# Kernel tuning notes

Hardware: AMD Instinct MI355X
Metric: run time of the kernel (lower is better)

Reference implementation:

```python
import jax, jax.numpy as jnp
import numpy as np

B, K, D, TPE, PPE, HEADS = 8, 128, 128, 64, 64, 8


def setup_inputs() -> dict:
    key = jax.random.key(0)
    ks = jax.random.split(key, 16)
    rn = lambda i, s: jax.random.normal(ks[i], s, dtype=jnp.float32)
    w = lambda i, s: rn(i, s) * 0.05
    z = lambda n: jnp.zeros((n,), jnp.float32)
    return {
        "v_f": rn(0, (B, K, D)),
        "e_f": rn(1, (B, K * K, D)),
        "p_pe": rn(2, (B, K, PPE)),
        "t_pe": rn(3, (B, TPE)),
        "W_vpe": w(4, (D + PPE + TPE, D)), "b_vpe": z(D),
        "W_epe": w(5, (D + TPE, D)), "b_epe": z(D),
        "W_ev1": w(6, (D + 2 * D, D)), "b_ev1": z(D),
        "W_ev2": w(7, (D, D)), "b_ev2": z(D),
        "W_q": w(8, (D, D)), "b_q": z(D),
        "W_k": w(9, (D, D)), "b_k": z(D),
        "W_self": w(10, (D, D)), "b_self": z(D),
        "W_out": w(11, (2 * D, D)), "b_out": z(D),
    }


def reference(v_f, e_f, p_pe, t_pe, W_vpe, b_vpe, W_epe, b_epe, W_ev1, b_ev1,
              W_ev2, b_ev2, W_q, b_q, W_k, b_k, W_self, b_self, W_out, b_out):
    silu = jax.nn.silu
    Bv, Kv, _ = v_f.shape
    t_dim = t_pe.shape[-1]
    # PE binding MLPs
    t_v = jnp.broadcast_to(t_pe[:, None, :], (Bv, Kv, t_dim))
    v = silu(jnp.concatenate([v_f, p_pe, t_v], -1) @ W_vpe + b_vpe)  # [B,K,D]
    t_e = jnp.broadcast_to(t_pe[:, None, :], (Bv, Kv * Kv, t_dim))
    e = silu(jnp.concatenate([e_f, t_e], -1) @ W_epe + b_epe)        # [B,K*K,D]
    Dv = v.shape[-1]
    # pairwise node features + edge feature -> edge value MLP
    e_mtx = e.reshape(Bv, Kv, Kv, -1)
    ev = jnp.concatenate([
        jnp.broadcast_to(v[:, :, None, :], (Bv, Kv, Kv, Dv)),
        jnp.broadcast_to(v[:, None, :, :], (Bv, Kv, Kv, Dv)),
        e_mtx], -1)                                                   # [B,K,K,3D]
    e_value = silu(ev @ W_ev1 + b_ev1) @ W_ev2 + b_ev2                # [B,K,K,E]
    E = e_value.shape[-1]
    G = E // HEADS
    # grouped-head elementwise-QK attention, softmax over neighbor axis (2)
    q = v @ W_q + b_q
    k = v @ W_k + b_k
    scores = (q[:, :, None, :] * k[:, None, :, :]).reshape(Bv, Kv, Kv, G, HEADS)
    scores = scores.sum(-1) / np.float32(np.sqrt(HEADS * 3.0))        # [B,K,K,G]
    atten = jax.nn.softmax(scores, axis=2)
    agg = (atten[..., None] * e_value.reshape(Bv, Kv, Kv, G, HEADS)).sum(2)
    agg = agg.reshape(Bv, Kv, E)
    vf = agg + silu(v @ W_self + b_self)
    pool = jnp.broadcast_to(vf.max(axis=1, keepdims=True), vf.shape)
    v_out = silu(jnp.concatenate([vf, pool], -1) @ W_out + b_out)     # [B,K,Vout]
    return v_out, e_value.reshape(Bv, Kv * Kv, E)
```

## Files before the change

### kernel.cpp

```cpp
#include <hip/hip_runtime.h>
#include <hip/hip_bf16.h>


typedef __attribute__((ext_vector_type(8)))  short bh8;
typedef __attribute__((ext_vector_type(16))) float f16v;
typedef __attribute__((ext_vector_type(4)))  float f4v;

__device__ __forceinline__ unsigned short f2bf(float f) {
  unsigned u = __builtin_bit_cast(unsigned, f);
  u += 0x7fffu + ((u >> 16) & 1u);
  return (unsigned short)(u >> 16);
}
__device__ __forceinline__ float silu_f(float x) {
  float e = __builtin_amdgcn_exp2f(x * -1.44269504088896f);
  return x * __builtin_amdgcn_rcpf(1.f + e);
}
__device__ __forceinline__ bh8 cvt8(f4v x, f4v y) {
  bh8 a;
  a[0] = (short)f2bf(x[0]); a[1] = (short)f2bf(x[1]);
  a[2] = (short)f2bf(x[2]); a[3] = (short)f2bf(x[3]);
  a[4] = (short)f2bf(y[0]); a[5] = (short)f2bf(y[1]);
  a[6] = (short)f2bf(y[2]); a[7] = (short)f2bf(y[3]);
  return a;
}
typedef const __attribute__((address_space(1))) unsigned int gq_t;
typedef __attribute__((address_space(3))) unsigned int lq_t;
__device__ __forceinline__ void gload_lds16(const void* g, void* l) {
  __builtin_amdgcn_global_load_lds((gq_t*)g, (lq_t*)l, 16, 0, 0);
}

__device__ __forceinline__ void wfrag_work(const float* __restrict__ W,
                                           short* __restrict__ dst, int kdim,
                                           int blk, int nblk) {
  int ksteps = kdim >> 4;
  int total  = kdim * 128;
  for (int idx = blk * 256 + threadIdx.x; idx < total; idx += nblk * 256) {
    int jj = idx & 7;
    int l  = (idx >> 3) & 63;
    int rest = idx >> 9;
    int ks = rest % ksteps;
    int ni = rest / ksteps;
    int n  = ni * 32 + (l & 31);
    int kk = ks * 16 + ((l >> 5) << 3) + jj;
    dst[idx] = (short)f2bf(W[kk * 128 + n]);
  }
}

__global__ __launch_bounds__(256) void k_front(
    const float* __restrict__ W_epe, short* __restrict__ wf1,
    const float* __restrict__ W_ev1, short* __restrict__ wf2,
    const float* __restrict__ W_ev2, short* __restrict__ wf3,
    const float* __restrict__ tpe, const float* __restrict__ bepe,
    float* __restrict__ tc,
    const float* __restrict__ vfeat, const float* __restrict__ ppe,
    const float* __restrict__ Wv, const float* __restrict__ bv,
    const float* __restrict__ Wq, const float* __restrict__ bq,
    const float* __restrict__ Wk, const float* __restrict__ bk,
    const float* __restrict__ Ws, const float* __restrict__ bs,
    const float* __restrict__ We, const float* __restrict__ be,
    unsigned short* __restrict__ vb16, float* __restrict__ q,
    float* __restrict__ kb, float* __restrict__ sa, float* __restrict__ evi) {
  const int blk = blockIdx.x;
  if (blk < 260) {
    if (blk < 64)       wfrag_work(W_epe, wf1, 128, blk, 64);
    else if (blk < 192) wfrag_work(W_ev1 + 128 * 128, wf2, 256, blk - 64, 128);
    else if (blk < 256) wfrag_work(W_ev2, wf3, 128, blk - 192, 64);
    else {
      int t = threadIdx.x;
      int b = (blk - 256) * 2 + (t >> 7);
      int n = t & 127;
      float a = bepe[n];
      for (int k2 = 0; k2 < 64; ++k2)
        a += tpe[b * 64 + k2] * W_epe[(128 + k2) * 128 + n];
      tc[b * 128 + n] = a;
    }
    return;
  }
  __shared__ float x[4][256];
  __shared__ float par[2][4][128];
  __shared__ float xv[4][128];
  const int r0 = (blk - 260) * 4;
  const int b  = r0 >> 7;
  const int t  = threadIdx.x;
  const int c  = t & 127;
  const int hf = t >> 7;
  #pragma unroll
  for (int rr = 0; rr < 4; ++rr) {
    int row = r0 + rr;
    x[rr][t] = (t < 128) ? vfeat[row * 128 + t]
             : (t < 192) ? ppe[row * 64 + (t - 128)]
                         : tpe[b * 64 + (t - 192)];
  }
  __syncthreads();
  {
    float a0 = 0.f, a1 = 0.f, a2 = 0.f, a3 = 0.f;
    const int k0 = hf * 128;
    for (int k4 = k0; k4 < k0 + 128; k4 += 4) {
      f4v x0 = *(const f4v*)&x[0][k4];
      f4v x1 = *(const f4v*)&x[1][k4];
      f4v x2 = *(const f4v*)&x[2][k4];
      f4v x3 = *(const f4v*)&x[3][k4];
      #pragma unroll
      for (int u = 0; u < 4; ++u) {
        float wv = Wv[(k4 + u) * 128 + c];
        a0 += x0[u] * wv; a1 += x1[u] * wv; a2 += x2[u] * wv; a3 += x3[u] * wv;
      }
    }
    par[hf][0][c] = a0; par[hf][1][c] = a1; par[hf][2][c] = a2; par[hf][3][c] = a3;
  }
  __syncthreads();
  if (hf == 0) {
    const float bvv = bv[c];
    #pragma unroll
    for (int rr = 0; rr < 4; ++rr) {
      float s = silu_f(par[0][rr][c] + par[1][rr][c] + bvv);
      vb16[(r0 + rr) * 128 + c] = f2bf(s);
      xv[rr][c] = s;
    }
  }
  __syncthreads();
  const float* WA = hf ? Ws : Wq;
  const float* WB = hf ? We : Wk;
  const float  ba = hf ? bs[c] : bq[c];
  const float  bb = hf ? be[c] : bk[c];
  float aA[4] = {ba, ba, ba, ba}, aB[4] = {bb, bb, bb, bb};
  for (int k4 = 0; k4 < 128; k4 += 4) {
    f4v x0 = *(const f4v*)&xv[0][k4];
    f4v x1 = *(const f4v*)&xv[1][k4];
    f4v x2 = *(const f4v*)&xv[2][k4];
    f4v x3 = *(const f4v*)&xv[3][k4];
    #pragma unroll
    for (int u = 0; u < 4; ++u) {
      float wa = WA[(k4 + u) * 128 + c];
      float wb = WB[(k4 + u) * 128 + c];
      aA[0] += x0[u] * wa; aA[1] += x1[u] * wa; aA[2] += x2[u] * wa; aA[3] += x3[u] * wa;
      aB[0] += x0[u] * wb; aB[1] += x1[u] * wb; aB[2] += x2[u] * wb; aB[3] += x3[u] * wb;
    }
  }
  if (hf == 0) {
    #pragma unroll
    for (int rr = 0; rr < 4; ++rr) {
      q[(r0 + rr) * 128 + c]  = aA[rr];
      kb[(r0 + rr) * 128 + c] = aB[rr];
    }
  } else {
    #pragma unroll
    for (int rr = 0; rr < 4; ++rr) {
      sa[(r0 + rr) * 128 + c]  = silu_f(aA[rr]);
      evi[(r0 + rr) * 128 + c] = aB[rr];
    }
  }
}

__global__ void k_atten(const float* __restrict__ q, const float* __restrict__ kmat,
                        float* __restrict__ atten) {
  __shared__ float qr[128];
  __shared__ float s[128][17];
  __shared__ float red[8][17];
  __shared__ float gmax[16];
  __shared__ float gsum[16];
  const int bi = blockIdx.x;
  const int b  = bi >> 7;
  const int t  = threadIdx.x;
  qr[t] = q[bi * 128 + t];
  __syncthreads();
  const float sc = 0.20412414523193154f;
  float loc[16];
  const float* krow = kmat + (size_t)(b * 128 + t) * 128;
  #pragma unroll
  for (int g = 0; g < 16; ++g) {
    f4v k0 = *(const f4v*)&krow[g * 8];
    f4v k1 = *(const f4v*)&krow[g * 8 + 4];
    float a = 0.f;
    #pragma unroll
    for (int h = 0; h < 4; ++h) a += qr[g * 8 + h] * k0[h] + qr[g * 8 + 4 + h] * k1[h];
    loc[g] = a * sc;
    s[t][g] = loc[g];
  }
  __syncthreads();
  { int g = t & 15, c = t >> 4;
    float m = -1e30f;
    for (int j2 = c * 16; j2 < c * 16 + 16; ++j2) m = fmaxf(m, s[j2][g]);
    red[c][g] = m; }
  __syncthreads();
  if (t < 16) {
    float m = red[0][t];
    #pragma unroll
    for (int c = 1; c < 8; ++c) m = fmaxf(m, red[c][t]);
    gmax[t] = m;
  }
  __syncthreads();
  #pragma unroll
  for (int g = 0; g < 16; ++g) {
    loc[g] = __builtin_amdgcn_exp2f((loc[g] - gmax[g]) * 1.44269504088896f);
    s[t][g] = loc[g];
  }
  __syncthreads();
  { int g = t & 15, c = t >> 4;
    float m = 0.f;
    for (int j2 = c * 16; j2 < c * 16 + 16; ++j2) m += s[j2][g];
    red[c][g] = m; }
  __syncthreads();
  if (t < 16) {
    float m = 0.f;
    #pragma unroll
    for (int c = 0; c < 8; ++c) m += red[c][t];
    gsum[t] = m;
  }
  __syncthreads();
  float* ab = atten + (size_t)bi * 2048 + (size_t)t * 16;
  #pragma unroll
  for (int g = 0; g < 16; ++g) ab[g] = loc[g] * __builtin_amdgcn_rcpf(gsum[g]);
}

__global__ __launch_bounds__(256) void k_edge(
    const float* __restrict__ ef, const unsigned short* __restrict__ vb,
    const short* __restrict__ wf1, const short* __restrict__ wf2,
    const short* __restrict__ wf3, const float* __restrict__ tc,
    const float* __restrict__ evic, const float* __restrict__ bev2,
    const float* __restrict__ atten, const float* __restrict__ sab,
    float* __restrict__ oute, float* __restrict__ vfb) {
  __shared__ __align__(16) unsigned short wbuf0[4096];
  __shared__ __align__(16) unsigned short wbuf1[4096];
  __shared__ __align__(16) unsigned short hbuf[128 * 136];
  const int bi  = blockIdx.x;
  const int b   = bi >> 7;
  const int tid = threadIdx.x;
  const int w   = tid >> 6;
  const int l   = tid & 63;
  const int row = w * 32 + (l & 31);
  const int kh  = (l >> 5) << 3;
  const int cb  = l & 31;
  const int rb  = w * 32 + ((l >> 5) << 2);

  const float* efr = ef + (size_t)(bi * 128 + row) * 128;
  const unsigned short* vj = vb + (size_t)(b * 128 + row) * 128;

  auto stage2 = [&](const short* wfp, int KST, int kc, unsigned short* dstb) {
    #pragma unroll
    for (int it = 0; it < 2; ++it) {
      int g  = it * 4 + w;
      int ni = g & 3, kso = g >> 2;
      const short* src = wfp + ((size_t)(ni * KST + kc * 2 + kso) * 64 + l) * 8;
      gload_lds16(src, dstb + g * 512);
    }
  };
  f16v acc[4];
  auto compute2 = [&](const unsigned short* ws2, bh8 aa, bh8 ab2) {
    #pragma unroll
    for (int ni = 0; ni < 4; ++ni) {
      bh8 b0 = *(const bh8*)&ws2[ni * 512 + l * 8];
      acc[ni] = __builtin_amdgcn_mfma_f32_32x32x16_bf16(aa, b0, acc[ni], 0, 0, 0);
    }
    #pragma unroll
    for (int ni = 0; ni < 4; ++ni) {
      bh8 b1 = *(const bh8*)&ws2[(4 + ni) * 512 + l * 8];
      acc[ni] = __builtin_amdgcn_mfma_f32_32x32x16_bf16(ab2, b1, acc[ni], 0, 0, 0);
    }
  };
  auto ldA = [&](int t) -> bh8 {
    if (t < 8) {
      const float* p = efr + t * 16 + kh;
      f4v x0 = *(const f4v*)p;
      f4v x1 = *(const f4v*)(p + 4);
      return cvt8(x0, x1);
    } else if (t < 16) {
      return *(const bh8*)(vj + (t - 8) * 16 + kh);
    } else if (t < 24) {
      return *(const bh8*)&hbuf[row * 136 + (t - 16) * 16 + kh];
    } else {
      return *(const bh8*)&hbuf[row * 136 + (t - 24) * 16 + kh];
    }
  };

  float tin[4], ein[4];
  #pragma unroll
  for (int ni = 0; ni < 4; ++ni) {
    tin[ni] = tc[b * 128 + ni * 32 + cb];
    ein[ni] = evic[bi * 128 + ni * 32 + cb];
  }
  #pragma unroll
  for (int ni = 0; ni < 4; ++ni)
    #pragma unroll
    for (int r = 0; r < 16; ++r) acc[ni][r] = tin[ni];

  stage2(wf1, 8, 0, wbuf0);
  bh8 a0c = ldA(0), a1c = ldA(1);
  __syncthreads();

  #pragma unroll
  for (int c = 0; c < 16; ++c) {
    if (c + 1 < 16) {
      const short* wp; int KST, kc;
      if (c + 1 < 4)       { wp = wf1; KST = 8;  kc = c + 1; }
      else if (c + 1 < 12) { wp = wf2; KST = 16; kc = c + 1 - 4; }
      else                 { wp = wf3; KST = 8;  kc = c + 1 - 12; }
      stage2(wp, KST, kc, (c & 1) ? wbuf0 : wbuf1);
    }
    bh8 a0n, a1n;
    const bool pre = (c + 1 < 16) && (c != 11);
    if (pre) { a0n = ldA(2 * (c + 1)); a1n = ldA(2 * (c + 1) + 1); }
    compute2((c & 1) ? wbuf1 : wbuf0, a0c, a1c);
    if (c == 3) {
      #pragma unroll
      for (int ni = 0; ni < 4; ++ni) {
        int n = ni * 32 + cb;
        #pragma unroll
        for (int r = 0; r < 16; ++r) {
          int rj = rb + (r & 3) + ((r >> 2) << 3);
          hbuf[rj * 136 + n] = f2bf(silu_f(acc[ni][r]));
          acc[ni][r] = ein[ni];
        }
      }
    }
    if (c == 11) {
      #pragma unroll
      for (int ni = 0; ni < 4; ++ni) {
        int n = ni * 32 + cb;
        #pragma unroll
        for (int r = 0; r < 16; ++r) {
          int rj = rb + (r & 3) + ((r >> 2) << 3);
          hbuf[rj * 136 + n] = f2bf(silu_f(acc[ni][r]));
          acc[ni][r] = 0.f;
        }
      }
      a0c = ldA(24); a1c = ldA(25);
    } else if (pre) {
      a0c = a0n; a1c = a1n;
    }
    __syncthreads();
  }

  #pragma unroll
  for (int ni = 0; ni < 4; ++ni) {
    int n = ni * 32 + cb;
    float bv = bev2[n];
    #pragma unroll
    for (int r = 0; r < 16; ++r) {
      int rj = rb + (r & 3) + ((r >> 2) << 3);
      acc[ni][r] += bv;
      oute[(size_t)(bi * 128 + rj) * 128 + n] = acc[ni][r];
    }
  }

  __syncthreads();
  float* attf = (float*)hbuf;
  float* aggl = attf + 2048;
  const float* ap = atten + (size_t)bi * 2048;
  #pragma unroll
  for (int u = 0; u < 8; ++u) {
    int idx = u * 256 + tid;
    float v = ap[idx];
    int j2 = idx >> 4, g = idx & 15;
    attf[j2 * 16 + (g & 3) * 4 + (g >> 2)] = v;
  }
  float sav = 0.f;
  if (tid < 128) sav = sab[(size_t)bi * 128 + tid];
  __syncthreads();
  float p0 = 0.f, p1 = 0.f, p2 = 0.f, p3 = 0.f;
  const int gl = (l & 31) >> 3;
  #pragma unroll
  for (int r = 0; r < 16; ++r) {
    int rj = rb + (r & 3) + ((r >> 2) << 3);
    f4v av = *(const f4v*)&attf[rj * 16 + gl * 4];
    p0 += av[0] * acc[0][r]; p1 += av[1] * acc[1][r];
    p2 += av[2] * acc[2][r]; p3 += av[3] * acc[3][r];
  }
  p0 += __shfl_xor(p0, 32); p1 += __shfl_xor(p1, 32);
  p2 += __shfl_xor(p2, 32); p3 += __shfl_xor(p3, 32);
  if (l < 32) {
    aggl[w * 128 +  0 + l] = p0;
    aggl[w * 128 + 32 + l] = p1;
    aggl[w * 128 + 64 + l] = p2;
    aggl[w * 128 + 96 + l] = p3;
  }
  __syncthreads();
  if (tid < 128) {
    vfb[(size_t)bi * 128 + tid] =
        aggl[tid] + aggl[128 + tid] + aggl[256 + tid] + aggl[384 + tid] + sav;
  }
}

__global__ void k_pool(const float* __restrict__ vfb, float* __restrict__ pool) {
  const int b = blockIdx.x, t = threadIdx.x;
  float m0 = -1e30f, m1 = -1e30f, m2 = -1e30f, m3 = -1e30f;
  for (int i = 0; i < 128; i += 4) {
    m0 = fmaxf(m0, vfb[(size_t)(b * 128 + i + 0) * 128 + t]);
    m1 = fmaxf(m1, vfb[(size_t)(b * 128 + i + 1) * 128 + t]);
    m2 = fmaxf(m2, vfb[(size_t)(b * 128 + i + 2) * 128 + t]);
    m3 = fmaxf(m3, vfb[(size_t)(b * 128 + i + 3) * 128 + t]);
  }
  pool[b * 128 + t] = fmaxf(fmaxf(m0, m1), fmaxf(m2, m3));
}

__global__ __launch_bounds__(256) void k_out(
    const float* __restrict__ vfb, const float* __restrict__ pool,
    const float* __restrict__ W, const float* __restrict__ bias,
    float* __restrict__ vout) {
  __shared__ float x[4][256];
  __shared__ float par[2][4][128];
  const int r0 = blockIdx.x * 4;
  const int b  = r0 >> 7;
  const int t  = threadIdx.x;
  const int c  = t & 127;
  const int hf = t >> 7;
  #pragma unroll
  for (int rr = 0; rr < 4; ++rr)
    x[rr][t] = (t < 128) ? vfb[(r0 + rr) * 128 + t] : pool[b * 128 + (t - 128)];
  __syncthreads();
  {
    float a0 = 0.f, a1 = 0.f, a2 = 0.f, a3 = 0.f;
    const int k0 = hf * 128;
    for (int k4 = k0; k4 < k0 + 128; k4 += 4) {
      f4v x0 = *(const f4v*)&x[0][k4];
      f4v x1 = *(const f4v*)&x[1][k4];
      f4v x2 = *(const f4v*)&x[2][k4];
      f4v x3 = *(const f4v*)&x[3][k4];
      #pragma unroll
      for (int u = 0; u < 4; ++u) {
        float wv = W[(k4 + u) * 128 + c];
        a0 += x0[u] * wv; a1 += x1[u] * wv; a2 += x2[u] * wv; a3 += x3[u] * wv;
      }
    }
    par[hf][0][c] = a0; par[hf][1][c] = a1; par[hf][2][c] = a2; par[hf][3][c] = a3;
  }
  __syncthreads();
  if (hf == 0) {
    const float bvv = bias[c];
    #pragma unroll
    for (int rr = 0; rr < 4; ++rr)
      vout[(r0 + rr) * 128 + c] = silu_f(par[0][rr][c] + par[1][rr][c] + bvv);
  }
}

extern "C" void kernel_launch(void* const* d_in, const int* in_sizes, int n_in,
                              void* d_out, int out_size, void* d_ws, size_t ws_size,
                              hipStream_t stream) {
  const float* v_f    = (const float*)d_in[0];
  const float* e_f    = (const float*)d_in[1];
  const float* p_pe   = (const float*)d_in[2];
  const float* t_pe   = (const float*)d_in[3];
  const float* W_vpe  = (const float*)d_in[4];
  const float* b_vpe  = (const float*)d_in[5];
  const float* W_epe  = (const float*)d_in[6];
  const float* b_epe  = (const float*)d_in[7];
  const float* W_ev1  = (const float*)d_in[8];
  const float* b_ev1  = (const float*)d_in[9];
  const float* W_ev2  = (const float*)d_in[10];
  const float* b_ev2  = (const float*)d_in[11];
  const float* W_q    = (const float*)d_in[12];
  const float* b_q    = (const float*)d_in[13];
  const float* W_k    = (const float*)d_in[14];
  const float* b_k    = (const float*)d_in[15];
  const float* W_self = (const float*)d_in[16];
  const float* b_self = (const float*)d_in[17];
  const float* W_out  = (const float*)d_in[18];
  const float* b_out  = (const float*)d_in[19];

  char* ws = (char*)d_ws;
  unsigned short* vb16  = (unsigned short*)(ws + 0);
  float*          qbuf  = (float*)(ws + 262144);
  float*          kbuf  = (float*)(ws + 786432);
  float*          sabuf = (float*)(ws + 1310720);
  float*          vfbuf = (float*)(ws + 1835008);
  float*          evic  = (float*)(ws + 2359296);
  float*          pool  = (float*)(ws + 2883584);
  float*          tc    = (float*)(ws + 2887680);
  short*          wf1   = (short*)(ws + 2891776);
  short*          wf2   = (short*)(ws + 2924544);
  short*          wf3   = (short*)(ws + 2990080);
  float*          atten = (float*)(ws + 3022848);

  float* v_out = (float*)d_out;
  float* out_e = (float*)d_out + 131072;

  k_front<<<516, 256, 0, stream>>>(W_epe, wf1, W_ev1, wf2, W_ev2, wf3,
                                   t_pe, b_epe, tc,
                                   v_f, p_pe, W_vpe, b_vpe, W_q, b_q,
                                   W_k, b_k, W_self, b_self, W_ev1, b_ev1,
                                   vb16, qbuf, kbuf, sabuf, evic);
  k_atten<<<1024, 128, 0, stream>>>(qbuf, kbuf, atten);
  k_edge<<<1024, 256, 0, stream>>>(e_f, vb16, wf1, wf2, wf3, tc, evic,
                                   b_ev2, atten, sabuf, out_e, vfbuf);
  k_pool<<<8, 128, 0, stream>>>(vfbuf, pool);
  k_out<<<256, 256, 0, stream>>>(vfbuf, pool, W_out, b_out, v_out);
}
```

Baseline: 83.71 us.

## Fuse max-pool into edge kernel via atomic max, pack two rows per attention block

Removes the separate pooling kernel by having the edge kernel atomically max an order-preserving unsigned key of each node feature into a pool buffer, which is zeroed by an extra block in the front kernel. The attention kernel now handles two query rows per 256-thread block, halving its grid. The edge kernel's block index is remapped so consecutive blocks span different batches. This saves one launch and the pooling pass, at the cost of global atomics and an extra front block.

Result: faster. 81.69 us (-2.4%).

```diff
diff --git a/kernel.cpp b/kernel.cpp
--- a/kernel.cpp
+++ b/kernel.cpp
@@ -27,6 +27,14 @@
 typedef __attribute__((address_space(3))) unsigned int lq_t;
 __device__ __forceinline__ void gload_lds16(const void* g, void* l) {
   __builtin_amdgcn_global_load_lds((gq_t*)g, (lq_t*)l, 16, 0, 0);
+}
+__device__ __forceinline__ unsigned fkey(float x) {
+  unsigned u = __builtin_bit_cast(unsigned, x);
+  return u ^ (((unsigned)((int)u >> 31)) | 0x80000000u);
+}
+__device__ __forceinline__ float funkey(unsigned key) {
+  unsigned u = (key & 0x80000000u) ? (key ^ 0x80000000u) : ~key;
+  return __builtin_bit_cast(float, u);
 }
 
 __device__ __forceinline__ void wfrag_work(const float* __restrict__ W,
@@ -51,7 +59,7 @@
     const float* __restrict__ W_ev1, short* __restrict__ wf2,
     const float* __restrict__ W_ev2, short* __restrict__ wf3,
     const float* __restrict__ tpe, const float* __restrict__ bepe,
-    float* __restrict__ tc,
+    float* __restrict__ tc, unsigned* __restrict__ poolU,
     const float* __restrict__ vfeat, const float* __restrict__ ppe,
     const float* __restrict__ Wv, const float* __restrict__ bv,
     const float* __restrict__ Wq, const float* __restrict__ bq,
@@ -76,6 +84,10 @@
     }
     return;
   }
+  if (blk >= 516) {
+    for (int j = threadIdx.x; j < 1024; j += 256) poolU[j] = 0u;
+    return;
+  }
   __shared__ float x[4][256];
   __shared__ float par[2][4][128];
   __shared__ float xv[4][128];
@@ -152,65 +164,69 @@
   }
 }
 
-__global__ void k_atten(const float* __restrict__ q, const float* __restrict__ kmat,
-                        float* __restrict__ atten) {
-  __shared__ float qr[128];
-  __shared__ float s[128][17];
-  __shared__ float red[8][17];
-  __shared__ float gmax[16];
-  __shared__ float gsum[16];
-  const int bi = blockIdx.x;
-  const int b  = bi >> 7;
-  const int t  = threadIdx.x;
-  qr[t] = q[bi * 128 + t];
+__global__ __launch_bounds__(256) void k_atten(
+    const float* __restrict__ q, const float* __restrict__ kmat,
+    float* __restrict__ atten) {
+  __shared__ float qr[2][128];
+  __shared__ float s[2][128][17];
+  __shared__ float red[2][8][17];
+  __shared__ float gmax[2][16];
+  __shared__ float gsum[2][16];
+  const int tid = threadIdx.x;
+  const int hi  = tid >> 7;
+  const int tt  = tid & 127;
+  const int bi  = blockIdx.x * 2 + hi;
+  const int b   = bi >> 7;
+  qr[hi][tt] = q[(size_t)bi * 128 + tt];
   __syncthreads();
   const float sc = 0.20412414523193154f;
   float loc[16];
-  const float* krow = kmat + (size_t)(b * 128 + t) * 128;
+  const float* krow = kmat + (size_t)(b * 128 + tt) * 128;
   #pragma unroll
   for (int g = 0; g < 16; ++g) {
     f4v k0 = *(const f4v*)&krow[g * 8];
     f4v k1 = *(const f4v*)&krow[g * 8 + 4];
     float a = 0.f;
     #pragma unroll
-    for (int h = 0; h < 4; ++h) a += qr[g * 8 + h] * k0[h] + qr[g * 8 + 4 + h] * k1[h];
+    for (int h = 0; h < 4; ++h)
+      a += qr[hi][g * 8 + h] * k0[h] + qr[hi][g * 8 + 4 + h] * k1[h];
     loc[g] = a * sc;
-    s[t][g] = loc[g];
-  }
-  __syncthreads();
-  { int g = t & 15, c = t >> 4;
+    s[hi][tt][g] = loc[g];
+  }
+  __syncthreads();
+  { int g = tt & 15, c = tt >> 4;
     float m = -1e30f;
-    for (int j2 = c * 16; j2 < c * 16 + 16; ++j2) m = fmaxf(m, s[j2][g]);
-    red[c][g] = m; }
-  __syncthreads();
-  if (t < 16) {
-    float m = red[0][t];
-    #pragma unroll
-    for (int c = 1; c < 8; ++c) m = fmaxf(m, red[c][t]);
-    gmax[t] = m;
+    for (int j2 = c * 16; j2 < c * 16 + 16; ++j2) m = fmaxf(m, s[hi][j2][g]);
+    red[hi][c][g] = m; }
+  __syncthreads();
+  if (tt < 16) {
+    float m = red[hi][0][tt];
+    #pragma unroll
+    for (int c = 1; c < 8; ++c) m = fmaxf(m, red[hi][c][tt]);
+    gmax[hi][tt] = m;
   }
   __syncthreads();
   #pragma unroll
   for (int g = 0; g < 16; ++g) {
-    loc[g] = __builtin_amdgcn_exp2f((loc[g] - gmax[g]) * 1.44269504088896f);
-    s[t][g] = loc[g];
-  }
-  __syncthreads();
-  { int g = t & 15, c = t >> 4;
+    loc[g] = __builtin_amdgcn_exp2f((loc[g] - gmax[hi][g]) * 1.44269504088896f);
+    s[hi][tt][g] = loc[g];
+  }
+  __syncthreads();
+  { int g = tt & 15, c = tt >> 4;
     float m = 0.f;
-    for (int j2 = c * 16; j2 < c * 16 + 16; ++j2) m += s[j2][g];
-    red[c][g] = m; }
-  __syncthreads();
-  if (t < 16) {
+    for (int j2 = c * 16; j2 < c * 16 + 16; ++j2) m += s[hi][j2][g];
+    red[hi][c][g] = m; }
+  __syncthreads();
+  if (tt < 16) {
     float m = 0.f;
     #pragma unroll
-    for (int c = 0; c < 8; ++c) m += red[c][t];
-    gsum[t] = m;
-  }
-  __syncthreads();
-  float* ab = atten + (size_t)bi * 2048 + (size_t)t * 16;
-  #pragma unroll
-  for (int g = 0; g < 16; ++g) ab[g] = loc[g] * __builtin_amdgcn_rcpf(gsum[g]);
+    for (int c = 0; c < 8; ++c) m += red[hi][c][tt];
+    gsum[hi][tt] = m;
+  }
+  __syncthreads();
+  float* ab = atten + (size_t)bi * 2048 + (size_t)tt * 16;
+  #pragma unroll
+  for (int g = 0; g < 16; ++g) ab[g] = loc[g] * __builtin_amdgcn_rcpf(gsum[hi][g]);
 }
 
 __global__ __launch_bounds__(256) void k_edge(
@@ -219,11 +235,12 @@
     const short* __restrict__ wf3, const float* __restrict__ tc,
     const float* __restrict__ evic, const float* __restrict__ bev2,
     const float* __restrict__ atten, const float* __restrict__ sab,
-    float* __restrict__ oute, float* __restrict__ vfb) {
+    float* __restrict__ oute, float* __restrict__ vfb,
+    unsigned* __restrict__ poolU) {
   __shared__ __align__(16) unsigned short wbuf0[4096];
   __shared__ __align__(16) unsigned short wbuf1[4096];
   __shared__ __align__(16) unsigned short hbuf[128 * 136];
-  const int bi  = blockIdx.x;
+  const int bi  = ((blockIdx.x & 7) << 7) | (blockIdx.x >> 3);
   const int b   = bi >> 7;
   const int tid = threadIdx.x;
   const int w   = tid >> 6;
@@ -376,25 +393,14 @@
   }
   __syncthreads();
   if (tid < 128) {
-    vfb[(size_t)bi * 128 + tid] =
-        aggl[tid] + aggl[128 + tid] + aggl[256 + tid] + aggl[384 + tid] + sav;
-  }
-}
-
-__global__ void k_pool(const float* __restrict__ vfb, float* __restrict__ pool) {
-  const int b = blockIdx.x, t = threadIdx.x;
-  float m0 = -1e30f, m1 = -1e30f, m2 = -1e30f, m3 = -1e30f;
-  for (int i = 0; i < 128; i += 4) {
-    m0 = fmaxf(m0, vfb[(size_t)(b * 128 + i + 0) * 128 + t]);
-    m1 = fmaxf(m1, vfb[(size_t)(b * 128 + i + 1) * 128 + t]);
-    m2 = fmaxf(m2, vfb[(size_t)(b * 128 + i + 2) * 128 + t]);
-    m3 = fmaxf(m3, vfb[(size_t)(b * 128 + i + 3) * 128 + t]);
-  }
-  pool[b * 128 + t] = fmaxf(fmaxf(m0, m1), fmaxf(m2, m3));
+    float vf = aggl[tid] + aggl[128 + tid] + aggl[256 + tid] + aggl[384 + tid] + sav;
+    vfb[(size_t)bi * 128 + tid] = vf;
+    atomicMax(&poolU[b * 128 + tid], fkey(vf));
+  }
 }
 
 __global__ __launch_bounds__(256) void k_out(
-    const float* __restrict__ vfb, const float* __restrict__ pool,
+    const float* __restrict__ vfb, const unsigned* __restrict__ poolU,
     const float* __restrict__ W, const float* __restrict__ bias,
     float* __restrict__ vout) {
   __shared__ float x[4][256];
@@ -406,7 +412,8 @@
   const int hf = t >> 7;
   #pragma unroll
   for (int rr = 0; rr < 4; ++rr)
-    x[rr][t] = (t < 128) ? vfb[(r0 + rr) * 128 + t] : pool[b * 128 + (t - 128)];
+    x[rr][t] = (t < 128) ? vfb[(r0 + rr) * 128 + t]
+                         : funkey(poolU[b * 128 + (t - 128)]);
   __syncthreads();
   {
     float a0 = 0.f, a1 = 0.f, a2 = 0.f, a3 = 0.f;
@@ -464,7 +471,7 @@
   float*          sabuf = (float*)(ws + 1310720);
   float*          vfbuf = (float*)(ws + 1835008);
   float*          evic  = (float*)(ws + 2359296);
-  float*          pool  = (float*)(ws + 2883584);
+  unsigned*       poolU = (unsigned*)(ws + 2883584);
   float*          tc    = (float*)(ws + 2887680);
   short*          wf1   = (short*)(ws + 2891776);
   short*          wf2   = (short*)(ws + 2924544);
@@ -474,14 +481,13 @@
   float* v_out = (float*)d_out;
   float* out_e = (float*)d_out + 131072;
 
-  k_front<<<516, 256, 0, stream>>>(W_epe, wf1, W_ev1, wf2, W_ev2, wf3,
-                                   t_pe, b_epe, tc,
+  k_front<<<517, 256, 0, stream>>>(W_epe, wf1, W_ev1, wf2, W_ev2, wf3,
+                                   t_pe, b_epe, tc, poolU,
                                    v_f, p_pe, W_vpe, b_vpe, W_q, b_q,
                                    W_k, b_k, W_self, b_self, W_ev1, b_ev1,
                                    vb16, qbuf, kbuf, sabuf, evic);
-  k_atten<<<1024, 128, 0, stream>>>(qbuf, kbuf, atten);
+  k_atten<<<512, 256, 0, stream>>>(qbuf, kbuf, atten);
   k_edge<<<1024, 256, 0, stream>>>(e_f, vb16, wf1, wf2, wf3, tc, evic,
-                                   b_ev2, atten, sabuf, out_e, vfbuf);
-  k_pool<<<8, 128, 0, stream>>>(vfbuf, pool);
-  k_out<<<256, 256, 0, stream>>>(vfbuf, pool, W_out, b_out, v_out);
-}
+                                   b_ev2, atten, sabuf, out_e, vfbuf, poolU);
+  k_out<<<256, 256, 0, stream>>>(vfbuf, poolU, W_out, b_out, v_out);
+}
```
